# Kernel optimization log

Measured on AMD Instinct MI355X. Metric: run time of the kernel, lower is better.

Reference implementation:

```python
import jax, jax.numpy as jnp
import numpy as np

B, S, H, NH = 2, 2048, 1024, 16
D = H // NH

def setup_inputs() -> dict:
    key = jax.random.key(0)
    ks = jax.random.split(key, 9)
    s = 1.0 / np.sqrt(H)
    return {
        "x": jax.random.normal(ks[0], (B, S, H), jnp.float32),
        "wq": jax.random.uniform(ks[1], (H, H), jnp.float32, -s, s),
        "bq": jax.random.uniform(ks[2], (H,), jnp.float32, -s, s),
        "wk": jax.random.uniform(ks[3], (H, H), jnp.float32, -s, s),
        "bk": jax.random.uniform(ks[4], (H,), jnp.float32, -s, s),
        "wv": jax.random.uniform(ks[5], (H, H), jnp.float32, -s, s),
        "bv": jax.random.uniform(ks[6], (H,), jnp.float32, -s, s),
        "wo": jax.random.uniform(ks[7], (H, H), jnp.float32, -s, s),
        "bo": jax.random.uniform(ks[8], (H,), jnp.float32, -s, s),
    }

def _split_heads(t):
    # [B, S, H] -> [B, NH, S, D]
    return t.reshape(B, S, NH, D).transpose(0, 2, 1, 3)

def reference(x, wq, bq, wk, bk, wv, bv, wo, bo):
    q = _split_heads(x @ wq.T + bq)
    k = _split_heads(x @ wk.T + bk)
    v = _split_heads(x @ wv.T + bv)
    scores = jnp.einsum('bhqd,bhkd->bhqk', q, k) / jnp.sqrt(jnp.float32(D))
    attn = jax.nn.softmax(scores, axis=-1)  # full [B,NH,S,S] materialized as in source
    ctx = jnp.einsum('bhqk,bhkd->bhqd', attn, v)
    concat = ctx.transpose(0, 2, 1, 3).reshape(B, S, H)
    return concat @ wo.T + bo
```

## Files before the change

kernel.cpp:

```cpp
#include <hip/hip_runtime.h>
#include <cstdint>

typedef unsigned short u16;
typedef __attribute__((ext_vector_type(8))) short short8;
typedef __attribute__((ext_vector_type(4))) float f32x4;

#if __has_builtin(__builtin_amdgcn_exp2f)
#define EXP2F(x) __builtin_amdgcn_exp2f(x)
#else
#define EXP2F(x) exp2f(x)
#endif

__device__ inline u16 f2bf(float f) {
  union { float f; unsigned u; } v; v.f = f;
  unsigned u = v.u;
  return (u16)((u + 0x7fffu + ((u >> 16) & 1u)) >> 16);
}

__device__ inline unsigned pk2bf_fast(float a, float b) {
  union { float f; unsigned u; } ua, ub; ua.f = a; ub.f = b;
  return __builtin_amdgcn_perm(ub.u + 0x8000u, ua.u + 0x8000u, 0x07060302u);
}

__global__ __launch_bounds__(256) void cvt_kernel(
    const float* __restrict__ x,
    const float* __restrict__ wq, const float* __restrict__ wk,
    const float* __restrict__ wv, const float* __restrict__ wo,
    u16* __restrict__ xb, u16* __restrict__ wqb, u16* __restrict__ wkb,
    u16* __restrict__ wvb, u16* __restrict__ wob) {
  const int y = blockIdx.y;
  const int Q = 1 << 20;
  const float* src;
  u16* dst;
  if (y < 4)       { src = x + y * Q; dst = xb + y * Q; }
  else if (y == 4) { src = wq; dst = wqb; }
  else if (y == 5) { src = wk; dst = wkb; }
  else if (y == 6) { src = wv; dst = wvb; }
  else             { src = wo; dst = wob; }
  const int i = (blockIdx.x * 256 + threadIdx.x) * 8;
  float4 a = *(const float4*)(src + i);
  float4 b = *(const float4*)(src + i + 4);
  short8 o;
  o[0] = (short)f2bf(a.x); o[1] = (short)f2bf(a.y);
  o[2] = (short)f2bf(a.z); o[3] = (short)f2bf(a.w);
  o[4] = (short)f2bf(b.x); o[5] = (short)f2bf(b.y);
  o[6] = (short)f2bf(b.z); o[7] = (short)f2bf(b.w);
  *(short8*)(dst + i) = o;
}

__global__ __launch_bounds__(256) void gemm_qkv(
    const u16* __restrict__ xb,
    const u16* __restrict__ wqb, const u16* __restrict__ wkb, const u16* __restrict__ wvb,
    const float* __restrict__ bq, const float* __restrict__ bk, const float* __restrict__ bv,
    u16* __restrict__ qo, u16* __restrict__ ko, u16* __restrict__ vto) {
  const int z = blockIdx.z;
  const u16* W = (z == 0) ? wqb : (z == 1) ? wkb : wvb;
  const float* bias = (z == 0) ? bq : (z == 1) ? bk : bv;

  __shared__ u16 smem[18432];
  u16* As = smem;
  u16* Bs = smem + 8192;
  const int tid = threadIdx.x, lane = tid & 63;
  const int wid = tid >> 6, wm = wid >> 1, wn = wid & 1;
  const int l15 = lane & 15, lg = lane >> 4;
  const int m0 = blockIdx.y * 128, n0 = blockIdx.x * 128;

  f32x4 acc[4][4] = {};
  short8 areg[4], breg[4];

#pragma unroll
  for (int i = 0; i < 4; ++i) {
    int c = i * 256 + tid;
    areg[i] = *(const short8*)(xb + (m0 + (c >> 3)) * 1024 + (c & 7) * 8);
    breg[i] = *(const short8*)(W  + (n0 + (c >> 3)) * 1024 + (c & 7) * 8);
  }

  for (int k0 = 0; k0 < 1024; k0 += 64) {
    __syncthreads();
#pragma unroll
    for (int i = 0; i < 4; ++i) {
      int c = i * 256 + tid;
      *(short8*)(As + c * 8) = areg[i];
      *(short8*)(Bs + c * 8) = breg[i];
    }
    if (k0 < 960) {
#pragma unroll
      for (int i = 0; i < 4; ++i) {
        int c = i * 256 + tid;
        areg[i] = *(const short8*)(xb + (m0 + (c >> 3)) * 1024 + k0 + 64 + (c & 7) * 8);
        breg[i] = *(const short8*)(W  + (n0 + (c >> 3)) * 1024 + k0 + 64 + (c & 7) * 8);
      }
    }
    __syncthreads();
#pragma unroll
    for (int kk = 0; kk < 2; ++kk) {
      short8 af[4], bf[4];
#pragma unroll
      for (int mb = 0; mb < 4; ++mb)
        af[mb] = *(const short8*)(As + (wm * 64 + mb * 16 + l15) * 64 + kk * 32 + lg * 8);
#pragma unroll
      for (int nb = 0; nb < 4; ++nb)
        bf[nb] = *(const short8*)(Bs + (wn * 64 + nb * 16 + l15) * 64 + kk * 32 + lg * 8);
#pragma unroll
      for (int mb = 0; mb < 4; ++mb)
#pragma unroll
        for (int nb = 0; nb < 4; ++nb)
          acc[mb][nb] = __builtin_amdgcn_mfma_f32_16x16x32_bf16(af[mb], bf[nb], acc[mb][nb], 0, 0, 0);
    }
  }

  if (z < 2) {
    u16* out = (z == 0) ? qo : ko;
#pragma unroll
    for (int mb = 0; mb < 4; ++mb)
#pragma unroll
      for (int nb = 0; nb < 4; ++nb)
#pragma unroll
        for (int r = 0; r < 4; ++r) {
          int m = m0 + wm * 64 + mb * 16 + lg * 4 + r;
          int n = n0 + wn * 64 + nb * 16 + l15;
          float v = acc[mb][nb][r] + bias[n];
          int b = m >> 11, s = m & 2047, h = n >> 6, d = n & 63;
          out[((b * 16 + h) * 2048 + s) * 64 + d] = f2bf(v);
        }
  } else {
    __syncthreads();
    u16* wbuf = smem + wid * 4608;
#pragma unroll
    for (int mb = 0; mb < 4; ++mb)
#pragma unroll
      for (int nb = 0; nb < 4; ++nb) {
        int n = n0 + wn * 64 + nb * 16 + l15;
        float bn = bias[n];
        int dl = nb * 16 + l15;
#pragma unroll
        for (int r = 0; r < 4; ++r) {
          int sig = (lg * 4 + r) * 4 + mb;
          wbuf[dl * 72 + sig] = f2bf(acc[mb][nb][r] + bn);
        }
      }
    int h_w = (n0 >> 6) + wn;
    int mbase = m0 + wm * 64;
    int b = mbase >> 11, sb = mbase & 2047;
#pragma unroll
    for (int i = 0; i < 8; ++i) {
      int dl = (lane >> 3) + 8 * i;
      int c = lane & 7;
      short8 vv = *(const short8*)(wbuf + dl * 72 + c * 8);
      *(short8*)(vto + ((b * 16 + h_w) * 64 + dl) * 2048 + sb + c * 8) = vv;
    }
  }
}

__global__ __launch_bounds__(256, 2) void attn_kernel(
    const u16* __restrict__ qg, const u16* __restrict__ kg,
    const u16* __restrict__ vtg, u16* __restrict__ ctxg) {
  const int h = blockIdx.x, qt = blockIdx.y, b = blockIdx.z;
  const int bh = b * 16 + h;
  const u16* Qg = qg + (bh * 2048 + qt * 128) * 64;
  const u16* Kg = kg + bh * 2048 * 64;
  const u16* Vg = vtg + bh * 64 * 2048;

  __shared__ u16 SP[128 * 72];
  __shared__ u16 Ks[64 * 72];
  __shared__ u16 Vts[64 * 72];

  const int tid = threadIdx.x, lane = tid & 63, wid = tid >> 6;
  const int l15 = lane & 15, lg = lane >> 4;
  const int row0 = wid * 32;

  short8 qf[2][2];
#pragma unroll
  for (int mb = 0; mb < 2; ++mb)
#pragma unroll
    for (int kk = 0; kk < 2; ++kk)
      qf[mb][kk] = *(const short8*)(Qg + (row0 + mb * 16 + l15) * 64 + kk * 32 + lg * 8);

  short8 ones8;
#pragma unroll
  for (int j = 0; j < 8; ++j) ones8[j] = (short)0x3F80;

  short8 kreg[2], vreg[2];
#pragma unroll
  for (int i = 0; i < 2; ++i) {
    int c = i * 256 + tid;
    kreg[i] = *(const short8*)(Kg + c * 8);
    vreg[i] = *(const short8*)(Vg + (c >> 3) * 2048 + (c & 7) * 8);
  }

  f32x4 acc[2][5] = {};
  const float cexp = 0.18033688011112042f;

  for (int kt = 0; kt < 32; ++kt) {
    __syncthreads();
#pragma unroll
    for (int i = 0; i < 2; ++i) {
      int c = i * 256 + tid;
      *(short8*)(Ks  + (c >> 3) * 72 + (c & 7) * 8) = kreg[i];
      *(short8*)(Vts + (c >> 3) * 72 + (c & 7) * 8) = vreg[i];
    }
    {
      const int ktn = (kt + 1 < 32) ? kt + 1 : 0;
#pragma unroll
      for (int i = 0; i < 2; ++i) {
        int c = i * 256 + tid;
        kreg[i] = *(const short8*)(Kg + ktn * 4096 + c * 8);
        vreg[i] = *(const short8*)(Vg + (c >> 3) * 2048 + ktn * 64 + (c & 7) * 8);
      }
    }
    __syncthreads();

    f32x4 sc[2][4] = {};
#pragma unroll
    for (int kk = 0; kk < 2; ++kk) {
      short8 bfr[4];
#pragma unroll
      for (int nb = 0; nb < 4; ++nb)
        bfr[nb] = *(const short8*)(Ks + (nb * 16 + l15) * 72 + kk * 32 + lg * 8);
#pragma unroll
      for (int mb = 0; mb < 2; ++mb)
#pragma unroll
        for (int nb = 0; nb < 4; ++nb)
          sc[mb][nb] = __builtin_amdgcn_mfma_f32_16x16x32_bf16(qf[mb][kk], bfr[nb], sc[mb][nb], 0, 0, 0);
    }

#pragma unroll
    for (int mb = 0; mb < 2; ++mb)
#pragma unroll
      for (int r = 0; r < 4; ++r) {
        float p0 = EXP2F(fmaf(sc[mb][0][r], cexp, -4.0f));
        float p1 = EXP2F(fmaf(sc[mb][1][r], cexp, -4.0f));
        float p2 = EXP2F(fmaf(sc[mb][2][r], cexp, -4.0f));
        float p3 = EXP2F(fmaf(sc[mb][3][r], cexp, -4.0f));
        uint2 u;
        u.x = pk2bf_fast(p0, p1);
        u.y = pk2bf_fast(p2, p3);
        *(uint2*)(SP + (row0 + mb * 16 + lg * 4 + r) * 72 + l15 * 4) = u;
      }

#pragma unroll
    for (int kk = 0; kk < 2; ++kk) {
      short8 pa[2], vb[4];
#pragma unroll
      for (int mb = 0; mb < 2; ++mb)
        pa[mb] = *(const short8*)(SP + (row0 + mb * 16 + l15) * 72 + kk * 32 + lg * 8);
#pragma unroll
      for (int nd = 0; nd < 4; ++nd)
        vb[nd] = *(const short8*)(Vts + (nd * 16 + l15) * 72 + kk * 32 + lg * 8);
#pragma unroll
      for (int mb = 0; mb < 2; ++mb) {
#pragma unroll
        for (int nd = 0; nd < 4; ++nd)
          acc[mb][nd] = __builtin_amdgcn_mfma_f32_16x16x32_bf16(pa[mb], vb[nd], acc[mb][nd], 0, 0, 0);
        acc[mb][4] = __builtin_amdgcn_mfma_f32_16x16x32_bf16(pa[mb], ones8, acc[mb][4], 0, 0, 0);
      }
    }
  }

#pragma unroll
  for (int mb = 0; mb < 2; ++mb)
#pragma unroll
    for (int r = 0; r < 4; ++r) {
      float inv = 1.0f / acc[mb][4][r];
      int s = qt * 128 + row0 + mb * 16 + lg * 4 + r;
      u16* dst = ctxg + (b * 2048 + s) * 1024 + h * 64;
#pragma unroll
      for (int nd = 0; nd < 4; ++nd)
        dst[nd * 16 + l15] = f2bf(acc[mb][nd][r] * inv);
    }
}

__global__ __launch_bounds__(256) void gemm_out(
    const u16* __restrict__ cb, const u16* __restrict__ wob,
    const float* __restrict__ bo, float* __restrict__ out) {
  __shared__ u16 As[128 * 64];
  __shared__ u16 Bs[64 * 64];
  const int tid = threadIdx.x, lane = tid & 63;
  const int wid = tid >> 6;
  const int l15 = lane & 15, lg = lane >> 4;
  const int m0 = blockIdx.y * 128, n0 = blockIdx.x * 64;

  f32x4 acc[2][4] = {};
  short8 areg[4], breg[2];

#pragma unroll
  for (int i = 0; i < 4; ++i) {
    int c = i * 256 + tid;
    areg[i] = *(const short8*)(cb + (m0 + (c >> 3)) * 1024 + (c & 7) * 8);
  }
#pragma unroll
  for (int i = 0; i < 2; ++i) {
    int c = i * 256 + tid;
    breg[i] = *(const short8*)(wob + (n0 + (c >> 3)) * 1024 + (c & 7) * 8);
  }

  for (int k0 = 0; k0 < 1024; k0 += 64) {
    __syncthreads();
#pragma unroll
    for (int i = 0; i < 4; ++i) {
      int c = i * 256 + tid;
      *(short8*)(As + c * 8) = areg[i];
    }
#pragma unroll
    for (int i = 0; i < 2; ++i) {
      int c = i * 256 + tid;
      *(short8*)(Bs + c * 8) = breg[i];
    }
    if (k0 < 960) {
#pragma unroll
      for (int i = 0; i < 4; ++i) {
        int c = i * 256 + tid;
        areg[i] = *(const short8*)(cb + (m0 + (c >> 3)) * 1024 + k0 + 64 + (c & 7) * 8);
      }
#pragma unroll
      for (int i = 0; i < 2; ++i) {
        int c = i * 256 + tid;
        breg[i] = *(const short8*)(wob + (n0 + (c >> 3)) * 1024 + k0 + 64 + (c & 7) * 8);
      }
    }
    __syncthreads();
#pragma unroll
    for (int kk = 0; kk < 2; ++kk) {
      short8 af[2], bf[4];
#pragma unroll
      for (int mb = 0; mb < 2; ++mb)
        af[mb] = *(const short8*)(As + (wid * 32 + mb * 16 + l15) * 64 + kk * 32 + lg * 8);
#pragma unroll
      for (int nb = 0; nb < 4; ++nb)
        bf[nb] = *(const short8*)(Bs + (nb * 16 + l15) * 64 + kk * 32 + lg * 8);
#pragma unroll
      for (int mb = 0; mb < 2; ++mb)
#pragma unroll
        for (int nb = 0; nb < 4; ++nb)
          acc[mb][nb] = __builtin_amdgcn_mfma_f32_16x16x32_bf16(af[mb], bf[nb], acc[mb][nb], 0, 0, 0);
    }
  }

#pragma unroll
  for (int mb = 0; mb < 2; ++mb)
#pragma unroll
    for (int nb = 0; nb < 4; ++nb)
#pragma unroll
      for (int r = 0; r < 4; ++r) {
        int m = m0 + wid * 32 + mb * 16 + lg * 4 + r;
        int n = n0 + nb * 16 + l15;
        out[m * 1024 + n] = acc[mb][nb][r] + bo[n];
      }
}

extern "C" void kernel_launch(void* const* d_in, const int* in_sizes, int n_in,
                              void* d_out, int out_size, void* d_ws, size_t ws_size,
                              hipStream_t stream) {
  const float* x  = (const float*)d_in[0];
  const float* wq = (const float*)d_in[1];
  const float* bq = (const float*)d_in[2];
  const float* wk = (const float*)d_in[3];
  const float* bk = (const float*)d_in[4];
  const float* wv = (const float*)d_in[5];
  const float* bv = (const float*)d_in[6];
  const float* wo = (const float*)d_in[7];
  const float* bo = (const float*)d_in[8];

  if (ws_size < (size_t)24 * 1024 * 1024 * 2) return;
  u16* xb   = (u16*)d_ws;
  u16* wqb  = xb  + (4u << 20);
  u16* wkb  = wqb + (1u << 20);
  u16* wvb  = wkb + (1u << 20);
  u16* wob  = wvb + (1u << 20);
  u16* qb   = wob + (1u << 20);
  u16* kb   = qb  + (4u << 20);
  u16* vtb  = kb  + (4u << 20);
  u16* ctxb = vtb + (4u << 20);

  cvt_kernel<<<dim3(512, 8, 1), 256, 0, stream>>>(x, wq, wk, wv, wo, xb, wqb, wkb, wvb, wob);
  gemm_qkv<<<dim3(8, 32, 3), 256, 0, stream>>>(xb, wqb, wkb, wvb, bq, bk, bv, qb, kb, vtb);
  attn_kernel<<<dim3(16, 16, 2), 256, 0, stream>>>(qb, kb, vtb, ctxb);
  gemm_out<<<dim3(16, 32, 1), 256, 0, stream>>>(ctxb, wob, bo, (float*)d_out);
}
```

Baseline: 205.6 us.

## Stream tiles straight to LDS with double buffering and XOR-swizzled producer layouts

Replaces the register-staged global-to-LDS copies in the QKV GEMM, attention and output GEMM with direct global_load_lds transfers into double-buffered shared memory. This removes one barrier per iteration and the VGPR round trip. To keep LDS reads conflict-free without padding, the conversion kernel, QKV epilogue and attention epilogue write x, the weights, K, V^T and ctx in an XOR-swizzled column order. Consumers apply the matching swizzle on their fragment reads. The cost is a larger LDS footprint, which may lower occupancy (64KB in gemm_qkv), and correctness now depends on every producer and consumer agreeing on the swizzle and on the async loads completing before the barrier.

```diff
diff --git a/kernel.cpp b/kernel.cpp
--- a/kernel.cpp
+++ b/kernel.cpp
@@ -21,6 +21,14 @@
   union { float f; unsigned u; } ua, ub; ua.f = a; ub.f = b;
   return __builtin_amdgcn_perm(ub.u + 0x8000u, ua.u + 0x8000u, 0x07060302u);
 }
+
+__device__ inline void gl2lds16(const void* g, void* l) {
+  __builtin_amdgcn_global_load_lds(
+      (const __attribute__((address_space(1))) unsigned int*)(unsigned long long)(uintptr_t)g,
+      (__attribute__((address_space(3))) unsigned int*)(unsigned int)(uintptr_t)l,
+      16, 0, 0);
+}
+
 
 __global__ __launch_bounds__(256) void cvt_kernel(
     const float* __restrict__ x,
@@ -45,7 +53,8 @@
   o[2] = (short)f2bf(a.z); o[3] = (short)f2bf(a.w);
   o[4] = (short)f2bf(b.x); o[5] = (short)f2bf(b.y);
   o[6] = (short)f2bf(b.z); o[7] = (short)f2bf(b.w);
-  *(short8*)(dst + i) = o;
+  const int j = (i & ~63) | (((((i >> 3) & 7) ^ ((i >> 10) & 7))) << 3);
+  *(short8*)(dst + j) = o;
 }
 
 __global__ __launch_bounds__(256) void gemm_qkv(
@@ -57,50 +66,48 @@
   const u16* W = (z == 0) ? wqb : (z == 1) ? wkb : wvb;
   const float* bias = (z == 0) ? bq : (z == 1) ? bk : bv;
 
-  __shared__ u16 smem[18432];
+  __shared__ u16 smem[32768];
   u16* As = smem;
-  u16* Bs = smem + 8192;
+  u16* Bs = smem + 16384;
   const int tid = threadIdx.x, lane = tid & 63;
   const int wid = tid >> 6, wm = wid >> 1, wn = wid & 1;
   const int l15 = lane & 15, lg = lane >> 4;
   const int m0 = blockIdx.y * 128, n0 = blockIdx.x * 128;
+  const int sw = ((l15 & 7) << 3);
 
   f32x4 acc[4][4] = {};
-  short8 areg[4], breg[4];
 
 #pragma unroll
   for (int i = 0; i < 4; ++i) {
     int c = i * 256 + tid;
-    areg[i] = *(const short8*)(xb + (m0 + (c >> 3)) * 1024 + (c & 7) * 8);
-    breg[i] = *(const short8*)(W  + (n0 + (c >> 3)) * 1024 + (c & 7) * 8);
+    gl2lds16(xb + (m0 + (c >> 3)) * 1024 + (c & 7) * 8, As + c * 8);
+    gl2lds16(W  + (n0 + (c >> 3)) * 1024 + (c & 7) * 8, Bs + c * 8);
   }
 
   for (int k0 = 0; k0 < 1024; k0 += 64) {
+    const int p = (k0 >> 6) & 1;
     __syncthreads();
-#pragma unroll
-    for (int i = 0; i < 4; ++i) {
-      int c = i * 256 + tid;
-      *(short8*)(As + c * 8) = areg[i];
-      *(short8*)(Bs + c * 8) = breg[i];
-    }
     if (k0 < 960) {
+      u16* An = As + (1 - p) * 8192;
+      u16* Bn = Bs + (1 - p) * 8192;
 #pragma unroll
       for (int i = 0; i < 4; ++i) {
         int c = i * 256 + tid;
-        areg[i] = *(const short8*)(xb + (m0 + (c >> 3)) * 1024 + k0 + 64 + (c & 7) * 8);
-        breg[i] = *(const short8*)(W  + (n0 + (c >> 3)) * 1024 + k0 + 64 + (c & 7) * 8);
-      }
-    }
-    __syncthreads();
+        gl2lds16(xb + (m0 + (c >> 3)) * 1024 + k0 + 64 + (c & 7) * 8, An + c * 8);
+        gl2lds16(W  + (n0 + (c >> 3)) * 1024 + k0 + 64 + (c & 7) * 8, Bn + c * 8);
+      }
+    }
+    const u16* Ap = As + p * 8192;
+    const u16* Bp = Bs + p * 8192;
 #pragma unroll
     for (int kk = 0; kk < 2; ++kk) {
       short8 af[4], bf[4];
 #pragma unroll
       for (int mb = 0; mb < 4; ++mb)
-        af[mb] = *(const short8*)(As + (wm * 64 + mb * 16 + l15) * 64 + kk * 32 + lg * 8);
+        af[mb] = *(const short8*)(Ap + (wm * 64 + mb * 16 + l15) * 64 + ((((kk * 4 + lg) << 3) ^ sw)));
 #pragma unroll
       for (int nb = 0; nb < 4; ++nb)
-        bf[nb] = *(const short8*)(Bs + (wn * 64 + nb * 16 + l15) * 64 + kk * 32 + lg * 8);
+        bf[nb] = *(const short8*)(Bp + (wn * 64 + nb * 16 + l15) * 64 + ((((kk * 4 + lg) << 3) ^ sw)));
 #pragma unroll
       for (int mb = 0; mb < 4; ++mb)
 #pragma unroll
@@ -120,8 +127,9 @@
           int m = m0 + wm * 64 + mb * 16 + lg * 4 + r;
           int n = n0 + wn * 64 + nb * 16 + l15;
           float v = acc[mb][nb][r] + bias[n];
-          int b = m >> 11, s = m & 2047, h = n >> 6, d = n & 63;
-          out[((b * 16 + h) * 2048 + s) * 64 + d] = f2bf(v);
+          int b = m >> 11, s = m & 2047, hh = n >> 6, d = n & 63;
+          int dcol = (z == 0) ? d : ((((d >> 3) ^ (s & 7)) << 3) | (d & 7));
+          out[((b * 16 + hh) * 2048 + s) * 64 + dcol] = f2bf(v);
         }
   } else {
     __syncthreads();
@@ -147,7 +155,8 @@
       int dl = (lane >> 3) + 8 * i;
       int c = lane & 7;
       short8 vv = *(const short8*)(wbuf + dl * 72 + c * 8);
-      *(short8*)(vto + ((b * 16 + h_w) * 64 + dl) * 2048 + sb + c * 8) = vv;
+      int cs = c ^ (dl & 7);
+      *(short8*)(vto + ((b * 16 + h_w) * 64 + dl) * 2048 + sb + cs * 8) = vv;
     }
   }
 }
@@ -162,12 +171,12 @@
   const u16* Vg = vtg + bh * 64 * 2048;
 
   __shared__ u16 SP[128 * 72];
-  __shared__ u16 Ks[64 * 72];
-  __shared__ u16 Vts[64 * 72];
+  __shared__ u16 KV[2][8192];
 
   const int tid = threadIdx.x, lane = tid & 63, wid = tid >> 6;
   const int l15 = lane & 15, lg = lane >> 4;
   const int row0 = wid * 32;
+  const int sw = ((l15 & 7) << 3);
 
   short8 qf[2][2];
 #pragma unroll
@@ -180,35 +189,29 @@
 #pragma unroll
   for (int j = 0; j < 8; ++j) ones8[j] = (short)0x3F80;
 
-  short8 kreg[2], vreg[2];
 #pragma unroll
   for (int i = 0; i < 2; ++i) {
     int c = i * 256 + tid;
-    kreg[i] = *(const short8*)(Kg + c * 8);
-    vreg[i] = *(const short8*)(Vg + (c >> 3) * 2048 + (c & 7) * 8);
+    gl2lds16(Kg + c * 8, &KV[0][c * 8]);
+    gl2lds16(Vg + (c >> 3) * 2048 + (c & 7) * 8, &KV[0][4096 + c * 8]);
   }
 
   f32x4 acc[2][5] = {};
   const float cexp = 0.18033688011112042f;
 
   for (int kt = 0; kt < 32; ++kt) {
+    const int p = kt & 1;
     __syncthreads();
-#pragma unroll
-    for (int i = 0; i < 2; ++i) {
-      int c = i * 256 + tid;
-      *(short8*)(Ks  + (c >> 3) * 72 + (c & 7) * 8) = kreg[i];
-      *(short8*)(Vts + (c >> 3) * 72 + (c & 7) * 8) = vreg[i];
-    }
-    {
-      const int ktn = (kt + 1 < 32) ? kt + 1 : 0;
+    if (kt < 31) {
 #pragma unroll
       for (int i = 0; i < 2; ++i) {
         int c = i * 256 + tid;
-        kreg[i] = *(const short8*)(Kg + ktn * 4096 + c * 8);
-        vreg[i] = *(const short8*)(Vg + (c >> 3) * 2048 + ktn * 64 + (c & 7) * 8);
-      }
-    }
-    __syncthreads();
+        gl2lds16(Kg + (kt + 1) * 4096 + c * 8, &KV[1 - p][c * 8]);
+        gl2lds16(Vg + (c >> 3) * 2048 + (kt + 1) * 64 + (c & 7) * 8, &KV[1 - p][4096 + c * 8]);
+      }
+    }
+    const u16* Ks = &KV[p][0];
+    const u16* Vts = &KV[p][4096];
 
     f32x4 sc[2][4] = {};
 #pragma unroll
@@ -216,7 +219,7 @@
       short8 bfr[4];
 #pragma unroll
       for (int nb = 0; nb < 4; ++nb)
-        bfr[nb] = *(const short8*)(Ks + (nb * 16 + l15) * 72 + kk * 32 + lg * 8);
+        bfr[nb] = *(const short8*)(Ks + (nb * 16 + l15) * 64 + ((((kk * 4 + lg) << 3)) ^ sw));
 #pragma unroll
       for (int mb = 0; mb < 2; ++mb)
 #pragma unroll
@@ -246,7 +249,7 @@
         pa[mb] = *(const short8*)(SP + (row0 + mb * 16 + l15) * 72 + kk * 32 + lg * 8);
 #pragma unroll
       for (int nd = 0; nd < 4; ++nd)
-        vb[nd] = *(const short8*)(Vts + (nd * 16 + l15) * 72 + kk * 32 + lg * 8);
+        vb[nd] = *(const short8*)(Vts + (nd * 16 + l15) * 64 + ((((kk * 4 + lg) << 3)) ^ sw));
 #pragma unroll
       for (int mb = 0; mb < 2; ++mb) {
 #pragma unroll
@@ -263,71 +266,70 @@
     for (int r = 0; r < 4; ++r) {
       float inv = 1.0f / acc[mb][4][r];
       int s = qt * 128 + row0 + mb * 16 + lg * 4 + r;
+      int s7 = s & 7;
       u16* dst = ctxg + (b * 2048 + s) * 1024 + h * 64;
 #pragma unroll
-      for (int nd = 0; nd < 4; ++nd)
-        dst[nd * 16 + l15] = f2bf(acc[mb][nd][r] * inv);
+      for (int nd = 0; nd < 4; ++nd) {
+        int d = nd * 16 + l15;
+        int dcol = (((d >> 3) ^ s7) << 3) | (d & 7);
+        dst[dcol] = f2bf(acc[mb][nd][r] * inv);
+      }
     }
 }
 
 __global__ __launch_bounds__(256) void gemm_out(
     const u16* __restrict__ cb, const u16* __restrict__ wob,
     const float* __restrict__ bo, float* __restrict__ out) {
-  __shared__ u16 As[128 * 64];
-  __shared__ u16 Bs[64 * 64];
+  __shared__ u16 smem[24576];
+  u16* As = smem;
+  u16* Bs = smem + 16384;
   const int tid = threadIdx.x, lane = tid & 63;
   const int wid = tid >> 6;
   const int l15 = lane & 15, lg = lane >> 4;
   const int m0 = blockIdx.y * 128, n0 = blockIdx.x * 64;
+  const int sw = ((l15 & 7) << 3);
 
   f32x4 acc[2][4] = {};
-  short8 areg[4], breg[2];
 
 #pragma unroll
   for (int i = 0; i < 4; ++i) {
     int c = i * 256 + tid;
-    areg[i] = *(const short8*)(cb + (m0 + (c >> 3)) * 1024 + (c & 7) * 8);
+    gl2lds16(cb + (m0 + (c >> 3)) * 1024 + (c & 7) * 8, As + c * 8);
   }
 #pragma unroll
   for (int i = 0; i < 2; ++i) {
     int c = i * 256 + tid;
-    breg[i] = *(const short8*)(wob + (n0 + (c >> 3)) * 1024 + (c & 7) * 8);
+    gl2lds16(wob + (n0 + (c >> 3)) * 1024 + (c & 7) * 8, Bs + c * 8);
   }
 
   for (int k0 = 0; k0 < 1024; k0 += 64) {
+    const int p = (k0 >> 6) & 1;
     __syncthreads();
-#pragma unroll
-    for (int i = 0; i < 4; ++i) {
-      int c = i * 256 + tid;
-      *(short8*)(As + c * 8) = areg[i];
-    }
-#pragma unroll
-    for (int i = 0; i < 2; ++i) {
-      int c = i * 256 + tid;
-      *(short8*)(Bs + c * 8) = breg[i];
-    }
     if (k0 < 960) {
+      u16* An = As + (1 - p) * 8192;
+      u16* Bn = Bs + (1 - p) * 4096;
 #pragma unroll
       for (int i = 0; i < 4; ++i) {
         int c = i * 256 + tid;
-        areg[i] = *(const short8*)(cb + (m0 + (c >> 3)) * 1024 + k0 + 64 + (c & 7) * 8);
+        gl2lds16(cb + (m0 + (c >> 3)) * 1024 + k0 + 64 + (c & 7) * 8, An + c * 8);
       }
 #pragma unroll
       for (int i = 0; i < 2; ++i) {
         int c = i * 256 + tid;
-        breg[i] = *(const short8*)(wob + (n0 + (c >> 3)) * 1024 + k0 + 64 + (c & 7) * 8);
-      }
-    }
-    __syncthreads();
+        gl2lds16(wob + (n0 + (c >> 3)) * 1024 + k0 + 64 + (c & 7) * 8, Bn + c * 8);
+      }
+    }
+    const u16* Ap = As + p * 8192;
+    const u16* Bp = Bs + p * 4096;
 #pragma unroll
     for (int kk = 0; kk < 2; ++kk) {
       short8 af[2], bf[4];
 #pragma unroll
       for (int mb = 0; mb < 2; ++mb)
-        af[mb] = *(const short8*)(As + (wid * 32 + mb * 16 + l15) * 64 + kk * 32 + lg * 8);
+        af[mb] = *(const short8*)(Ap + (wid * 32 + mb * 16 + l15) * 64 + ((((kk * 4 + lg) << 3)) ^ sw));
 #pragma unroll
       for (int nb = 0; nb < 4; ++nb)
-        bf[nb] = *(const short8*)(Bs + (nb * 16 + l15) * 64 + kk * 32 + lg * 8);
+        bf[nb] = *(const short8*)(Bp + (nb * 16 + l15) * 64 + ((((kk * 4 + lg) << 3)) ^ sw));
 #pragma unroll
       for (int mb = 0; mb < 2; ++mb)
 #pragma unroll
```

Result: faster. 190.0 us (-7.6%).
